# Kernel optimization log

Hardware: AMD Instinct MI355X
Metric: run time of the kernel (lower is better)

The kernel has to match this reference:

```python
import jax, jax.numpy as jnp
import numpy as np

B, Z, H, T = 256, 512, 2048, 16
EPS = 1e-5

def _normalize(v):
    return v / (jnp.linalg.norm(v) + 1e-12)

def setup_inputs() -> dict:
    key = jax.random.key(0)
    ks = jax.random.split(key, 10)
    s = lambda fan: 1.0 / np.sqrt(fan)
    return {
        "z": jax.random.normal(ks[0], (B, Z), dtype=jnp.float32),
        "fc_w": jax.random.normal(ks[1], (Z, Z), dtype=jnp.float32) * s(Z),
        "fc_b": jnp.zeros((Z,), dtype=jnp.float32),
        "fc_u": _normalize(jax.random.normal(ks[2], (Z,), dtype=jnp.float32)),
        "w_ih": jax.random.normal(ks[3], (3 * H, Z), dtype=jnp.float32) * s(Z),
        "w_hh": jax.random.normal(ks[4], (3 * H, H), dtype=jnp.float32) * s(H),
        "b_ih": jnp.zeros((3 * H,), dtype=jnp.float32).at[H:2 * H].set(1.0),  # forget-gate bias init
        "b_hh": jnp.zeros((3 * H,), dtype=jnp.float32),
        "lin_w": jax.random.normal(ks[5], (Z, H), dtype=jnp.float32) * s(H),
        "lin_b": jnp.zeros((Z,), dtype=jnp.float32),
    }

def _spectral_norm(w, u):
    # one torch-style power iteration (u, v treated as constants)
    v = jax.lax.stop_gradient(_normalize(w.T @ u))
    u1 = jax.lax.stop_gradient(_normalize(w @ v))
    sigma = u1 @ (w @ v)
    return w / sigma

def reference(z, fc_w, fc_b, fc_u, w_ih, w_hh, b_ih, b_hh, lin_w, lin_b):
    # spectral-norm linear: h0 = z @ (W/sigma)^T + b
    w_sn = _spectral_norm(fc_w, fc_u)
    x0 = z @ w_sn.T + fc_b                      # [B, Z]
    h0 = jnp.zeros((B, H), dtype=z.dtype)       # initHidden

    def step(carry, _):
        x, h = carry
        gi = x @ w_ih.T + b_ih                  # [B, 3H]
        gh = h @ w_hh.T + b_hh                  # [B, 3H]
        i_r, i_z, i_n = jnp.split(gi, 3, axis=1)
        h_r, h_z, h_n = jnp.split(gh, 3, axis=1)
        r = jax.nn.sigmoid(i_r + h_r)
        u = jax.nn.sigmoid(i_z + h_z)
        n = jnp.tanh(i_n + r * h_n)
        h_new = (1.0 - u) * n + u * h
        x_new = h_new @ lin_w.T + lin_b         # [B, Z] fed back as next input
        return (x_new, h_new), x_new

    _, outs = jax.lax.scan(step, (x0, h0), None, length=T)  # [T, B, Z]

    # per-timestep BatchNorm1d(affine=False), training-mode batch stats
    mean = jnp.mean(outs, axis=1, keepdims=True)
    var = jnp.mean((outs - mean) ** 2, axis=1, keepdims=True)
    y = (outs - mean) / jnp.sqrt(var + EPS)     # [T, B, Z]

    y = jnp.transpose(y, (1, 0, 2))             # [B, T, Z]
    return y.reshape(-1, Z)                     # [B*T, Z]
```

## Files before the change

kernel.cpp:

```cpp
#include <hip/hip_runtime.h>
#include <hip/hip_bf16.h>
#include <cstdint>
#include <cstddef>

#define B_  256
#define Z_  512
#define H_  2048
#define T_  16
#define H3_ 6144

using short8  = __attribute__((ext_vector_type(8))) short;
using bf16x8  = __attribute__((ext_vector_type(8))) __bf16;
using f32x4   = __attribute__((ext_vector_type(4))) float;
using f32x16  = __attribute__((ext_vector_type(16))) float;

__device__ __forceinline__ f32x4 mfma_bf16(short8 a, short8 b, f32x4 c) {
  return __builtin_amdgcn_mfma_f32_16x16x32_bf16(
      __builtin_bit_cast(bf16x8, a), __builtin_bit_cast(bf16x8, b), c, 0, 0, 0);
}
__device__ __forceinline__ f32x16 mfma_bf16_32(short8 a, short8 b, f32x16 c) {
  return __builtin_amdgcn_mfma_f32_32x32x16_bf16(
      __builtin_bit_cast(bf16x8, a), __builtin_bit_cast(bf16x8, b), c, 0, 0, 0);
}

__device__ __forceinline__ unsigned short f2bf(float f) {
  unsigned int u = __builtin_bit_cast(unsigned int, f);
  u = (u + 0x7FFFu + ((u >> 16) & 1u)) >> 16;
  return (unsigned short)u;
}

__device__ __forceinline__ float sigmoidf_(float x) { return 1.0f / (1.0f + __expf(-x)); }

__device__ __forceinline__ int swz(int row, int chunk) {
  return row * 64 + ((chunk ^ (row & 7)) << 3);
}

__global__ __launch_bounds__(512, 1) void gru_step4(
    const unsigned short* __restrict__ A, int K,
    const unsigned short* __restrict__ Wr,
    const unsigned short* __restrict__ Wz,
    const unsigned short* __restrict__ Wn,
    const unsigned short* __restrict__ Whn,
    const float* __restrict__ cr, const float* __restrict__ cz,
    const float* __restrict__ cn, const float* __restrict__ chn,
    float hn_scale,
    const float* __restrict__ h_old,
    float* __restrict__ h_new,
    unsigned short* __restrict__ h_hist)
{
  __shared__ __align__(16) unsigned short sbuf[2][12288];
  __shared__ float LDSf[4][64][33];
  const int bid = blockIdx.x, tid = threadIdx.x;
  const int xcd = bid & 7, rst = bid >> 3;
  const int m_idx = rst & 3, gg = rst >> 2;
  const int grp = gg * 8 + xcd;
  const int m0 = m_idx * 64;
  const int gh0 = grp * 32;
  const int wave = tid >> 6, lane = tid & 63;
  const int gate = wave & 3, mh = wave >> 2;
  const int lh = lane >> 5, l31 = lane & 31;

  const int arow = tid >> 3, achk = tid & 7;
  const int wrow = tid >> 2, wc0 = (tid & 3) * 2;
  const unsigned short* wsrc =
      (wrow < 32) ? Wr : (wrow < 64) ? Wz : (wrow < 96) ? Wn : Whn;
  const size_t aoff = (size_t)(m0 + arow) * K + achk * 8;
  const size_t woff = (size_t)(gh0 + (wrow & 31)) * K + wc0 * 8;
  const int sa_d  = swz(arow, achk);
  const int sw_d0 = 4096 + swz(wrow, wc0 + 0);
  const int sw_d1 = 4096 + swz(wrow, wc0 + 1);

  uint4 Aa, Aw0, Aw1;
  uint4 Ba, Bw0, Bw1;

#define LDSET(a, w0, w1, k0)                               \
  {                                                        \
    const int kk_ = (k0);                                  \
    a  = *(const uint4*)(A    + aoff + kk_);               \
    w0 = *(const uint4*)(wsrc + woff + kk_);               \
    w1 = *(const uint4*)(wsrc + woff + kk_ + 8);           \
  }
#define STAGE(s, a, w0, w1)                                \
  {                                                        \
    unsigned short* b_ = sbuf[s];                          \
    *(uint4*)(b_ + sa_d)  = a;                             \
    *(uint4*)(b_ + sw_d0) = w0;                            \
    *(uint4*)(b_ + sw_d1) = w1;                            \
  }

  f32x16 acc = {};
#define COMP(s)                                                            \
  {                                                                        \
    const unsigned short* b_ = sbuf[s];                                    \
    _Pragma("unroll")                                                      \
    for (int ks = 0; ks < 4; ++ks) {                                       \
      short8 af = *(const short8*)(b_ + swz(mh * 32 + l31, ks * 2 + lh));  \
      short8 wf = *(const short8*)(b_ + 4096 + swz(gate * 32 + l31, ks * 2 + lh)); \
      acc = mfma_bf16_32(af, wf, acc);                                     \
    }                                                                      \
  }

  const int nIter = K >> 6;
  LDSET(Aa, Aw0, Aw1, 0);
  LDSET(Ba, Bw0, Bw1, 64);
  for (int it = 0; it < nIter; it += 2) {
    STAGE(0, Aa, Aw0, Aw1);
    __syncthreads();
    { const int kn = (it + 2 < nIter) ? ((it + 2) << 6) : 0;
      LDSET(Aa, Aw0, Aw1, kn); }
    COMP(0);
    STAGE(1, Ba, Bw0, Bw1);
    __syncthreads();
    { const int kn = (it + 3 < nIter) ? ((it + 3) << 6) : 64;
      LDSET(Ba, Bw0, Bw1, kn); }
    COMP(1);
  }
#undef LDSET
#undef STAGE
#undef COMP

#pragma unroll
  for (int reg = 0; reg < 16; ++reg) {
    const int trow = (reg & 3) + 8 * (reg >> 2) + 4 * lh;
    LDSf[gate][mh * 32 + trow][l31] = acc[reg];
  }
  __syncthreads();
  {
    const int row = tid >> 3, c0 = (tid & 7) * 4;
    const int grow = m0 + row;
#pragma unroll
    for (int j = 0; j < 4; ++j) {
      const int col = c0 + j;
      const int gcol = gh0 + col;
      const float R   = sigmoidf_(LDSf[0][row][col] + cr[gcol]);
      const float U   = sigmoidf_(LDSf[1][row][col] + cz[gcol]);
      const float HNv = hn_scale * LDSf[3][row][col] + chn[gcol];
      const float Nv  = tanhf(LDSf[2][row][col] + cn[gcol] + R * HNv);
      const float ho  = h_old ? h_old[(size_t)grow * H_ + gcol] : 0.0f;
      const float hv  = (1.0f - U) * Nv + U * ho;
      h_new[(size_t)grow * H_ + gcol]  = hv;
      h_hist[(size_t)grow * H_ + gcol] = f2bf(hv);
    }
  }
}

__global__ __launch_bounds__(256) void gemm_bt(
    const unsigned short* __restrict__ A,
    const unsigned short* __restrict__ Bw,
    int K,
    const float* __restrict__ addsrc, int add_ld,
    const float* __restrict__ bias,
    const float* __restrict__ scale_ptr,
    unsigned short* __restrict__ out_bf,
    float* __restrict__ out_f, int ldo)
{
  __shared__ unsigned short sA[32 * 64];
  __shared__ unsigned short sB[64 * 64];
  const int tid  = threadIdx.x;
  const int m0   = blockIdx.x * 32, n0 = blockIdx.y * 64;
  const int wave = tid >> 6, lane = tid & 63;
  const int wr = wave & 1, wc = wave >> 1;
  const int q = lane >> 4, c16 = lane & 15;
  const int lr = tid >> 3, lc8 = tid & 7;
  f32x4 acc0 = {}, acc1 = {};
  const size_t rowA  = (size_t)(m0 + lr) * K;
  const size_t rowB0 = (size_t)(n0 + lr) * K;
  const size_t rowB1 = (size_t)(n0 + 32 + lr) * K;
  for (int k0 = 0; k0 < K; k0 += 64) {
    const int gc = k0 + lc8 * 8;
    uint4 ra  = *(const uint4*)(A  + rowA  + gc);
    uint4 rb0 = *(const uint4*)(Bw + rowB0 + gc);
    uint4 rb1 = *(const uint4*)(Bw + rowB1 + gc);
    __syncthreads();
    *(uint4*)(sA + swz(lr, lc8))      = ra;
    *(uint4*)(sB + swz(lr, lc8))      = rb0;
    *(uint4*)(sB + swz(32 + lr, lc8)) = rb1;
    __syncthreads();
#pragma unroll
    for (int kk = 0; kk < 2; ++kk) {
      const int arow = wr * 16 + c16;
      short8 af = *(const short8*)(sA + swz(arow, kk * 4 + q));
      const int brow = wc * 32 + c16;
      short8 b0 = *(const short8*)(sB + swz(brow, kk * 4 + q));
      acc0 = mfma_bf16(af, b0, acc0);
      short8 b1 = *(const short8*)(sB + swz(brow + 16, kk * 4 + q));
      acc1 = mfma_bf16(af, b1, acc1);
    }
  }
  const float scale = scale_ptr ? *scale_ptr : 1.0f;
#pragma unroll
  for (int cf = 0; cf < 2; ++cf) {
    f32x4 a = cf ? acc1 : acc0;
#pragma unroll
    for (int v = 0; v < 4; ++v) {
      const int row = m0 + wr * 16 + q * 4 + v;
      const int col = n0 + wc * 32 + cf * 16 + c16;
      float val = a[v] * scale;
      if (addsrc) val += addsrc[(size_t)row * add_ld + col];
      if (bias)   val += bias[col];
      if (out_f)  out_f[(size_t)row * ldo + col] = val;
      if (out_bf) out_bf[(size_t)row * ldo + col] = f2bf(val);
    }
  }
}

__global__ __launch_bounds__(256) void gemm_bt64(
    const unsigned short* __restrict__ A,
    const unsigned short* __restrict__ Bw,
    int K,
    const float* __restrict__ addsrc, int add_ld,
    const float* __restrict__ bias,
    unsigned short* __restrict__ out_bf,
    float* __restrict__ out_f, int ldo)
{
  __shared__ unsigned short sA[64 * 64];
  __shared__ unsigned short sB[64 * 64];
  const int tid  = threadIdx.x;
  const int m0   = blockIdx.x * 64, n0 = blockIdx.y * 64;
  const int wave = tid >> 6, lane = tid & 63;
  const int wr = wave & 1, wc = wave >> 1;
  const int q = lane >> 4, c16 = lane & 15;
  const int lr = tid >> 3, lc8 = tid & 7;
  f32x4 acc[2][2] = {};
  const size_t aoff = (size_t)(m0 + lr) * K;
  const size_t boff = (size_t)(n0 + lr) * K;
  const size_t s32  = (size_t)32 * K;

  uint4 ra0, ra1, rb0, rb1;
  auto LOAD = [&](int k0) {
    const int gc = k0 + lc8 * 8;
    ra0 = *(const uint4*)(A  + aoff + gc);
    ra1 = *(const uint4*)(A  + aoff + s32 + gc);
    rb0 = *(const uint4*)(Bw + boff + gc);
    rb1 = *(const uint4*)(Bw + boff + s32 + gc);
  };

  const int nIter = K >> 6;
  LOAD(0);
  for (int it = 0; it < nIter; ++it) {
    __syncthreads();
    *(uint4*)(sA + swz(lr, lc8))      = ra0;
    *(uint4*)(sA + swz(lr + 32, lc8)) = ra1;
    *(uint4*)(sB + swz(lr, lc8))      = rb0;
    *(uint4*)(sB + swz(lr + 32, lc8)) = rb1;
    __syncthreads();
    if (it + 1 < nIter) LOAD((it + 1) << 6);
#pragma unroll
    for (int kk = 0; kk < 2; ++kk) {
      short8 af0 = *(const short8*)(sA + swz(wr * 32 + c16,      kk * 4 + q));
      short8 af1 = *(const short8*)(sA + swz(wr * 32 + 16 + c16, kk * 4 + q));
      short8 bf0 = *(const short8*)(sB + swz(wc * 32 + c16,      kk * 4 + q));
      short8 bf1 = *(const short8*)(sB + swz(wc * 32 + 16 + c16, kk * 4 + q));
      acc[0][0] = mfma_bf16(af0, bf0, acc[0][0]);
      acc[0][1] = mfma_bf16(af0, bf1, acc[0][1]);
      acc[1][0] = mfma_bf16(af1, bf0, acc[1][0]);
      acc[1][1] = mfma_bf16(af1, bf1, acc[1][1]);
    }
  }
#pragma unroll
  for (int i = 0; i < 2; ++i) {
#pragma unroll
    for (int j = 0; j < 2; ++j) {
#pragma unroll
      for (int v = 0; v < 4; ++v) {
        const int row = m0 + wr * 32 + i * 16 + q * 4 + v;
        const int col = n0 + wc * 32 + j * 16 + c16;
        float val = acc[i][j][v];
        if (addsrc) val += addsrc[(size_t)row * add_ld + col];
        if (bias)   val += bias[col];
        if (out_f)  out_f[(size_t)row * ldo + col] = val;
        if (out_bf) out_bf[(size_t)row * ldo + col] = f2bf(val);
      }
    }
  }
}

__global__ __launch_bounds__(256) void quant_all(
    const float* __restrict__ z, const float* __restrict__ fc_w,
    const float* __restrict__ w_ih, const float* __restrict__ w_hh,
    const float* __restrict__ lin_w,
    unsigned short* __restrict__ z_q, unsigned short* __restrict__ fc_w_q,
    unsigned short* __restrict__ w_ih_q, unsigned short* __restrict__ w_hhn_q,
    unsigned short* __restrict__ lin_w_q)
{
  const int i = blockIdx.x * 256 + threadIdx.x;
  if (i >= 2195456) return;
  const float4* src; ushort4* dst; int idx;
  if (i < 32768)        { src = (const float4*)z;     dst = (ushort4*)z_q;     idx = i; }
  else if (i < 98304)   { src = (const float4*)fc_w;  dst = (ushort4*)fc_w_q;  idx = i - 32768; }
  else if (i < 884736)  { src = (const float4*)w_ih;  dst = (ushort4*)w_ih_q;  idx = i - 98304; }
  else if (i < 1933312) { src = (const float4*)(w_hh + (size_t)2 * H_ * H_);
                          dst = (ushort4*)w_hhn_q;    idx = i - 884736; }
  else                  { src = (const float4*)lin_w; dst = (ushort4*)lin_w_q; idx = i - 1933312; }
  float4 v = src[idx];
  ushort4 o; o.x = f2bf(v.x); o.y = f2bf(v.y); o.z = f2bf(v.z); o.w = f2bf(v.w);
  dst[idx] = o;
}

__global__ __launch_bounds__(256) void transq(const float* __restrict__ s,
                                              unsigned short* __restrict__ d) {
  __shared__ float tile[32][33];
  const int tx = threadIdx.x & 31, ty = threadIdx.x >> 5;
  const int k0 = blockIdx.x * 32, z0 = blockIdx.y * 32;
#pragma unroll
  for (int j = 0; j < 4; ++j)
    tile[ty + j * 8][tx] = s[(size_t)(z0 + ty + j * 8) * H_ + k0 + tx];
  __syncthreads();
#pragma unroll
  for (int j = 0; j < 4; ++j)
    d[(size_t)(k0 + ty + j * 8) * Z_ + z0 + tx] = f2bf(tile[tx][ty + j * 8]);
}

__global__ void sigma1(const float* __restrict__ W, const float* __restrict__ u,
                       float* __restrict__ t1) {
  __shared__ float part[4][64];
  const int lane = threadIdx.x & 63, wv = threadIdx.x >> 6;
  const int col = blockIdx.x * 64 + lane;
  float s = 0.f;
  for (int r = wv * 128; r < wv * 128 + 128; ++r)
    s += W[(size_t)r * Z_ + col] * u[r];
  part[wv][lane] = s;
  __syncthreads();
  if (wv == 0)
    t1[col] = part[0][lane] + part[1][lane] + part[2][lane] + part[3][lane];
}

__global__ void sigma1b(const float* __restrict__ t1, float* __restrict__ invn) {
  __shared__ float red[256];
  int t = threadIdx.x;
  float v0 = t1[t], v1 = t1[t + 256];
  red[t] = v0 * v0 + v1 * v1;
  __syncthreads();
  for (int s = 128; s > 0; s >>= 1) {
    if (t < s) red[t] += red[t + s];
    __syncthreads();
  }
  if (t == 0) invn[0] = 1.0f / (sqrtf(red[0]) + 1e-12f);
}

__global__ void sigma2(const float* __restrict__ W, const float* __restrict__ t1,
                       const float* __restrict__ invn, float* __restrict__ t2) {
  const int lane = threadIdx.x & 63, wv = threadIdx.x >> 6;
  const int row = blockIdx.x * 4 + wv;
  float s = 0.f;
  for (int c = lane; c < Z_; c += 64) s += W[(size_t)row * Z_ + c] * t1[c];
#pragma unroll
  for (int off = 32; off > 0; off >>= 1) s += __shfl_down(s, off);
  if (lane == 0) t2[row] = s * invn[0];
}

__global__ void sigma3(const float* __restrict__ t2, float* __restrict__ inv_sig) {
  __shared__ float red[256];
  int t = threadIdx.x;
  float v0 = t2[t], v1 = t2[t + 256];
  red[t] = v0 * v0 + v1 * v1;
  __syncthreads();
  for (int s = 128; s > 0; s >>= 1) {
    if (t < s) red[t] += red[t + s];
    __syncthreads();
  }
  if (t == 0) {
    float s2  = red[0];
    float sig = s2 / (sqrtf(s2) + 1e-12f);
    inv_sig[0] = 1.0f / sig;
  }
}

__global__ __launch_bounds__(256) void dots_k(const float* __restrict__ w,
                                              const float* __restrict__ lb,
                                              float* __restrict__ dvec) {
  const int wave = threadIdx.x >> 6, lane = threadIdx.x & 63;
#pragma unroll
  for (int i = 0; i < 4; ++i) {
    int row = blockIdx.x * 16 + wave * 4 + i;
    float s = 0.f;
    for (int c = lane; c < Z_; c += 64) s += w[(size_t)row * Z_ + c] * lb[c];
#pragma unroll
    for (int off = 32; off > 0; off >>= 1) s += __shfl_down(s, off);
    if (lane == 0) dvec[row] = s;
  }
}

__global__ void consts_k(const float* __restrict__ b_ih, const float* __restrict__ b_hh,
                         const float* __restrict__ dvec,
                         float* __restrict__ c0r, float* __restrict__ c0z,
                         float* __restrict__ c0n,
                         float* __restrict__ c1r, float* __restrict__ c1z,
                         float* __restrict__ c1n, float* __restrict__ chn) {
  int j = blockIdx.x * 256 + threadIdx.x;
  float br = b_ih[j], bz = b_ih[H_ + j], bn = b_ih[2 * H_ + j];
  float hr = b_hh[j], hz = b_hh[H_ + j], hn = b_hh[2 * H_ + j];
  c0r[j] = br + hr; c0z[j] = bz + hz; c0n[j] = bn; chn[j] = hn;
  c1r[j] = br + hr + dvec[j];
  c1z[j] = bz + hz + dvec[H_ + j];
  c1n[j] = bn + dvec[2 * H_ + j];
}

__global__ __launch_bounds__(256) void bn_k(const float* __restrict__ outs,
                                            float* __restrict__ y) {
  __shared__ float s_sum[4][64], s_sq[4][64], s_mean[64], s_inv[64];
  const int t = blockIdx.x, zb = blockIdx.y;
  const int zl = threadIdx.x & 63, bp = threadIdx.x >> 6;
  const int z = zb * 64 + zl;
  float sum = 0.f, sq = 0.f;
  for (int b = bp * 64; b < bp * 64 + 64; ++b) {
    float v = outs[(size_t)(t * 256 + b) * Z_ + z];
    sum += v; sq += v * v;
  }
  s_sum[bp][zl] = sum; s_sq[bp][zl] = sq;
  __syncthreads();
  if (bp == 0) {
    float S = s_sum[0][zl] + s_sum[1][zl] + s_sum[2][zl] + s_sum[3][zl];
    float Q = s_sq[0][zl] + s_sq[1][zl] + s_sq[2][zl] + s_sq[3][zl];
    float mean = S * (1.0f / 256.0f);
    float var  = Q * (1.0f / 256.0f) - mean * mean;
    s_mean[zl] = mean;
    s_inv[zl]  = rsqrtf(var + 1e-5f);
  }
  __syncthreads();
  const float mean = s_mean[zl], inv = s_inv[zl];
  for (int b = bp * 64; b < bp * 64 + 64; ++b) {
    float v = outs[(size_t)(t * 256 + b) * Z_ + z];
    y[(size_t)(b * T_ + t) * Z_ + z] = (v - mean) * inv;
  }
}

extern "C" void kernel_launch(void* const* d_in, const int* in_sizes, int n_in,
                              void* d_out, int out_size, void* d_ws, size_t ws_size,
                              hipStream_t stream) {
  const float* z     = (const float*)d_in[0];
  const float* fc_w  = (const float*)d_in[1];
  const float* fc_b  = (const float*)d_in[2];
  const float* fc_u  = (const float*)d_in[3];
  const float* w_ih  = (const float*)d_in[4];
  const float* w_hh  = (const float*)d_in[5];
  const float* b_ih  = (const float*)d_in[6];
  const float* b_hh  = (const float*)d_in[7];
  const float* lin_w = (const float*)d_in[8];
  const float* lin_b = (const float*)d_in[9];
  float* out = (float*)d_out;

  char* ws = (char*)d_ws;
  size_t off = 0;
  auto alloc = [&](size_t bytes) -> void* {
    off = (off + 255) & ~(size_t)255;
    void* p = ws + off;
    off += bytes;
    return p;
  };
  unsigned short* w_ih_q   = (unsigned short*)alloc((size_t)H3_ * Z_ * 2);
  unsigned short* w_hhn_q  = (unsigned short*)alloc((size_t)H_ * H_ * 2);
  unsigned short* lin_w_q  = (unsigned short*)alloc((size_t)Z_ * H_ * 2);
  unsigned short* lin_wT_q = (unsigned short*)alloc((size_t)Z_ * H_ * 2);
  unsigned short* fc_w_q   = (unsigned short*)alloc((size_t)Z_ * Z_ * 2);
  unsigned short* z_q      = (unsigned short*)alloc((size_t)B_ * Z_ * 2);
  unsigned short* x0_q     = (unsigned short*)alloc((size_t)B_ * Z_ * 2);
  unsigned short* Wsum_r   = (unsigned short*)alloc((size_t)H_ * H_ * 2);
  unsigned short* Wsum_z   = (unsigned short*)alloc((size_t)H_ * H_ * 2);
  unsigned short* Wn_c     = (unsigned short*)alloc((size_t)H_ * H_ * 2);
  unsigned short* Hhist    = (unsigned short*)alloc((size_t)T_ * B_ * H_ * 2);
  float* h_f32 = (float*)alloc((size_t)2 * B_ * H_ * 4);
  float* outs  = (float*)alloc((size_t)T_ * B_ * Z_ * 4);
  float* c0r = (float*)alloc(H_ * 4);
  float* c0z = (float*)alloc(H_ * 4);
  float* c0n = (float*)alloc(H_ * 4);
  float* c1r = (float*)alloc(H_ * 4);
  float* c1z = (float*)alloc(H_ * 4);
  float* c1n = (float*)alloc(H_ * 4);
  float* chn = (float*)alloc(H_ * 4);
  float* dvec = (float*)alloc(H3_ * 4);
  float* t1v = (float*)alloc(Z_ * 4);
  float* t2v = (float*)alloc(Z_ * 4);
  float* invn = (float*)alloc(256);
  float* invsig = (float*)alloc(256);
  (void)in_sizes; (void)n_in; (void)out_size; (void)ws_size;

  quant_all<<<dim3((2195456 + 255) / 256), 256, 0, stream>>>(
      z, fc_w, w_ih, w_hh, lin_w, z_q, fc_w_q, w_ih_q, w_hhn_q, lin_w_q);
  transq<<<dim3(64, 16), 256, 0, stream>>>(lin_w, lin_wT_q);
  sigma1<<<8, 256, 0, stream>>>(fc_w, fc_u, t1v);
  sigma1b<<<1, 256, 0, stream>>>(t1v, invn);
  sigma2<<<128, 256, 0, stream>>>(fc_w, t1v, invn, t2v);
  sigma3<<<1, 256, 0, stream>>>(t2v, invsig);
  dots_k<<<384, 256, 0, stream>>>(w_ih, lin_b, dvec);
  consts_k<<<8, 256, 0, stream>>>(b_ih, b_hh, dvec, c0r, c0z, c0n, c1r, c1z, c1n, chn);

  gemm_bt<<<dim3(B_ / 32, Z_ / 64), 256, 0, stream>>>(
      z_q, fc_w_q, Z_, nullptr, 0, fc_b, invsig, x0_q, nullptr, Z_);

  for (int g = 0; g < 3; ++g) {
    const float* adds = (g < 2) ? (w_hh + (size_t)g * H_ * H_) : nullptr;
    unsigned short* outw = (g == 0) ? Wsum_r : (g == 1) ? Wsum_z : Wn_c;
    gemm_bt64<<<dim3(H_ / 64, H_ / 64), 256, 0, stream>>>(
        w_ih_q + (size_t)g * H_ * Z_, lin_wT_q, Z_, adds, H_, nullptr,
        outw, nullptr, H_);
  }

  for (int t = 0; t < T_; ++t) {
    if (t == 0) {
      gru_step4<<<256, 512, 0, stream>>>(
          x0_q, Z_,
          w_ih_q, w_ih_q + (size_t)H_ * Z_, w_ih_q + (size_t)2 * H_ * Z_,
          w_ih_q ,
          c0r, c0z, c0n, chn, 0.0f, nullptr, h_f32, Hhist);
    } else {
      gru_step4<<<256, 512, 0, stream>>>(
          Hhist + (size_t)(t - 1) * B_ * H_, H_,
          Wsum_r, Wsum_z, Wn_c, w_hhn_q,
          c1r, c1z, c1n, chn, 1.0f,
          h_f32 + (size_t)((t - 1) & 1) * B_ * H_,
          h_f32 + (size_t)(t & 1) * B_ * H_,
          Hhist + (size_t)t * B_ * H_);
    }
  }

  gemm_bt64<<<dim3(T_ * B_ / 64, Z_ / 64), 256, 0, stream>>>(
      Hhist, lin_w_q, H_, nullptr, 0, lin_b, nullptr, outs, Z_);

  bn_k<<<dim3(T_, Z_ / 64), 256, 0, stream>>>(outs, out);
}
```

Baseline: 402.9 us.

## Split-K GRU step with 2x2 MFMA tiles, merge weight-sum GEMMs and setup kernels

The per-step GRU kernel now gives each of four k-slices to a wave group. Each wave computes a 2x2 block of 32x32 MFMA tiles, so A and W fragments are reused within the wave, and a shared-memory reduction sums the partial results. The three weight-sum GEMMs become one launch with 128x128 tiles. The sigma and bias-constant setup kernels are merged to cut launch count. The split-K reduction adds extra LDS traffic and a shared buffer of 96KB plus staging, which raises LDS pressure in exchange for fewer redundant fragment loads.

```diff
diff --git a/kernel.cpp b/kernel.cpp
--- a/kernel.cpp
+++ b/kernel.cpp
@@ -35,7 +35,7 @@
   return row * 64 + ((chunk ^ (row & 7)) << 3);
 }
 
-__global__ __launch_bounds__(512, 1) void gru_step4(
+__global__ __launch_bounds__(512, 1) void gru_step7(
     const unsigned short* __restrict__ A, int K,
     const unsigned short* __restrict__ Wr,
     const unsigned short* __restrict__ Wz,
@@ -49,7 +49,8 @@
     unsigned short* __restrict__ h_hist)
 {
   __shared__ __align__(16) unsigned short sbuf[2][12288];
-  __shared__ float LDSf[4][64][33];
+  __shared__ float red[6][4096];
+  float* LDSf = (float*)sbuf;
   const int bid = blockIdx.x, tid = threadIdx.x;
   const int xcd = bid & 7, rst = bid >> 3;
   const int m_idx = rst & 3, gg = rst >> 2;
@@ -57,7 +58,7 @@
   const int m0 = m_idx * 64;
   const int gh0 = grp * 32;
   const int wave = tid >> 6, lane = tid & 63;
-  const int gate = wave & 3, mh = wave >> 2;
+  const int s4 = wave & 3, gp = wave >> 2;
   const int lh = lane >> 5, l31 = lane & 31;
 
   const int arow = tid >> 3, achk = tid & 7;
@@ -88,16 +89,21 @@
     *(uint4*)(b_ + sw_d1) = w1;                            \
   }
 
-  f32x16 acc = {};
-#define COMP(s)                                                            \
+  f32x16 a00 = {}, a01 = {}, a10 = {}, a11 = {};
+  const int g0r = gp * 64, g1r = gp * 64 + 32;
+
+#define COMP(sb)                                                           \
   {                                                                        \
-    const unsigned short* b_ = sbuf[s];                                    \
-    _Pragma("unroll")                                                      \
-    for (int ks = 0; ks < 4; ++ks) {                                       \
-      short8 af = *(const short8*)(b_ + swz(mh * 32 + l31, ks * 2 + lh));  \
-      short8 wf = *(const short8*)(b_ + 4096 + swz(gate * 32 + l31, ks * 2 + lh)); \
-      acc = mfma_bf16_32(af, wf, acc);                                     \
-    }                                                                      \
+    const unsigned short* b_ = sbuf[sb];                                   \
+    const int ch = s4 * 2 + lh;                                            \
+    short8 af0 = *(const short8*)(b_ + swz(l31, ch));                      \
+    short8 af1 = *(const short8*)(b_ + swz(32 + l31, ch));                 \
+    short8 wf0 = *(const short8*)(b_ + 4096 + swz(g0r + l31, ch));         \
+    short8 wf1 = *(const short8*)(b_ + 4096 + swz(g1r + l31, ch));         \
+    a00 = mfma_bf16_32(af0, wf0, a00);                                     \
+    a01 = mfma_bf16_32(af0, wf1, a01);                                     \
+    a10 = mfma_bf16_32(af1, wf0, a10);                                     \
+    a11 = mfma_bf16_32(af1, wf1, a11);                                     \
   }
 
   const int nIter = K >> 6;
@@ -119,10 +125,41 @@
 #undef STAGE
 #undef COMP
 
-#pragma unroll
-  for (int reg = 0; reg < 16; ++reg) {
-    const int trow = (reg & 3) + 8 * (reg >> 2) + 4 * lh;
-    LDSf[gate][mh * 32 + trow][l31] = acc[reg];
+  __syncthreads();
+  if (s4 != 0) {
+    float* rp = red[(s4 - 1) * 2 + gp];
+#pragma unroll
+    for (int r = 0; r < 16; ++r) rp[(0 * 16 + r) * 64 + lane] = a00[r];
+#pragma unroll
+    for (int r = 0; r < 16; ++r) rp[(1 * 16 + r) * 64 + lane] = a01[r];
+#pragma unroll
+    for (int r = 0; r < 16; ++r) rp[(2 * 16 + r) * 64 + lane] = a10[r];
+#pragma unroll
+    for (int r = 0; r < 16; ++r) rp[(3 * 16 + r) * 64 + lane] = a11[r];
+  }
+  __syncthreads();
+  if (s4 == 0) {
+#pragma unroll
+    for (int ss = 0; ss < 3; ++ss) {
+      const float* rp = red[ss * 2 + gp];
+#pragma unroll
+      for (int r = 0; r < 16; ++r) a00[r] += rp[(0 * 16 + r) * 64 + lane];
+#pragma unroll
+      for (int r = 0; r < 16; ++r) a01[r] += rp[(1 * 16 + r) * 64 + lane];
+#pragma unroll
+      for (int r = 0; r < 16; ++r) a10[r] += rp[(2 * 16 + r) * 64 + lane];
+#pragma unroll
+      for (int r = 0; r < 16; ++r) a11[r] += rp[(3 * 16 + r) * 64 + lane];
+    }
+    const int gA = gp * 2, gB = gp * 2 + 1;
+#pragma unroll
+    for (int r = 0; r < 16; ++r) {
+      const int trow = (r & 3) + 8 * (r >> 2) + 4 * lh;
+      LDSf[(gA * 64 + trow     ) * 33 + l31] = a00[r];
+      LDSf[(gB * 64 + trow     ) * 33 + l31] = a01[r];
+      LDSf[(gA * 64 + 32 + trow) * 33 + l31] = a10[r];
+      LDSf[(gB * 64 + 32 + trow) * 33 + l31] = a11[r];
+    }
   }
   __syncthreads();
   {
@@ -132,14 +169,88 @@
     for (int j = 0; j < 4; ++j) {
       const int col = c0 + j;
       const int gcol = gh0 + col;
-      const float R   = sigmoidf_(LDSf[0][row][col] + cr[gcol]);
-      const float U   = sigmoidf_(LDSf[1][row][col] + cz[gcol]);
-      const float HNv = hn_scale * LDSf[3][row][col] + chn[gcol];
-      const float Nv  = tanhf(LDSf[2][row][col] + cn[gcol] + R * HNv);
+      const float R   = sigmoidf_(LDSf[(0 * 64 + row) * 33 + col] + cr[gcol]);
+      const float U   = sigmoidf_(LDSf[(1 * 64 + row) * 33 + col] + cz[gcol]);
+      const float HNv = hn_scale * LDSf[(3 * 64 + row) * 33 + col] + chn[gcol];
+      const float Nv  = tanhf(LDSf[(2 * 64 + row) * 33 + col] + cn[gcol] + R * HNv);
       const float ho  = h_old ? h_old[(size_t)grow * H_ + gcol] : 0.0f;
       const float hv  = (1.0f - U) * Nv + U * ho;
       h_new[(size_t)grow * H_ + gcol]  = hv;
       h_hist[(size_t)grow * H_ + gcol] = f2bf(hv);
+    }
+  }
+}
+
+__global__ __launch_bounds__(512) void gemm128_wsum(
+    const unsigned short* __restrict__ w_ih_q,
+    const unsigned short* __restrict__ lin_wT_q,
+    const float* __restrict__ w_hh,
+    unsigned short* __restrict__ Wsum_r,
+    unsigned short* __restrict__ Wsum_z,
+    unsigned short* __restrict__ Wn_c)
+{
+  __shared__ __align__(16) unsigned short sA[2][8192];
+  __shared__ __align__(16) unsigned short sB[2][8192];
+  const int g = blockIdx.y >> 4, nj = blockIdx.y & 15;
+  const unsigned short* Aq = w_ih_q + (size_t)g * H_ * Z_;
+  const float* adds = (g < 2) ? (w_hh + (size_t)g * H_ * H_) : nullptr;
+  unsigned short* outw = (g == 0) ? Wsum_r : (g == 1) ? Wsum_z : Wn_c;
+  const int K = Z_;
+  const int m0 = blockIdx.x * 128, n0 = nj * 128;
+  const int tid = threadIdx.x;
+  const int wave = tid >> 6, lane = tid & 63;
+  const int wr = wave & 1, wc = wave >> 1;
+  const int lh = lane >> 5, l31 = lane & 31;
+  const int srow = tid >> 2, sc0 = (tid & 3) * 2;
+  const size_t aoff = (size_t)(m0 + srow) * K + sc0 * 8;
+  const size_t boff = (size_t)(n0 + srow) * K + sc0 * 8;
+  const int sd0 = swz(srow, sc0), sd1 = swz(srow, sc0 + 1);
+  f32x16 acc0 = {}, acc1 = {};
+  uint4 A0, A1, B0, B1, C0, C1, D0, D1;
+#define LD(a0, a1, b0, b1, k0)                              \
+  { const int kk_ = (k0);                                   \
+    a0 = *(const uint4*)(Aq + aoff + kk_);                  \
+    a1 = *(const uint4*)(Aq + aoff + kk_ + 8);              \
+    b0 = *(const uint4*)(lin_wT_q + boff + kk_);            \
+    b1 = *(const uint4*)(lin_wT_q + boff + kk_ + 8); }
+#define ST(s, a0, a1, b0, b1)                               \
+  { *(uint4*)(sA[s] + sd0) = a0; *(uint4*)(sA[s] + sd1) = a1; \
+    *(uint4*)(sB[s] + sd0) = b0; *(uint4*)(sB[s] + sd1) = b1; }
+#define CP(s)                                               \
+  { _Pragma("unroll")                                       \
+    for (int ks = 0; ks < 4; ++ks) {                        \
+      const int ch = ks * 2 + lh;                           \
+      short8 af0 = *(const short8*)(sA[s] + swz(wr * 64 + l31, ch));      \
+      short8 af1 = *(const short8*)(sA[s] + swz(wr * 64 + 32 + l31, ch)); \
+      short8 bf  = *(const short8*)(sB[s] + swz(wc * 32 + l31, ch));      \
+      acc0 = mfma_bf16_32(af0, bf, acc0);                   \
+      acc1 = mfma_bf16_32(af1, bf, acc1); } }
+  const int nIter = K >> 6;
+  LD(A0, A1, B0, B1, 0);
+  LD(C0, C1, D0, D1, 64);
+  for (int it = 0; it < nIter; it += 2) {
+    ST(0, A0, A1, B0, B1);
+    __syncthreads();
+    { const int kn = (it + 2 < nIter) ? ((it + 2) << 6) : 0; LD(A0, A1, B0, B1, kn); }
+    CP(0);
+    ST(1, C0, C1, D0, D1);
+    __syncthreads();
+    { const int kn = (it + 3 < nIter) ? ((it + 3) << 6) : 64; LD(C0, C1, D0, D1, kn); }
+    CP(1);
+  }
+#undef LD
+#undef ST
+#undef CP
+#pragma unroll
+  for (int i = 0; i < 2; ++i) {
+    const f32x16 a = i ? acc1 : acc0;
+#pragma unroll
+    for (int r = 0; r < 16; ++r) {
+      const int row = m0 + wr * 64 + i * 32 + (r & 3) + 8 * (r >> 2) + 4 * lh;
+      const int col = n0 + wc * 32 + l31;
+      float val = a[r];
+      if (adds) val += adds[(size_t)row * H_ + col];
+      outw[(size_t)row * H_ + col] = f2bf(val);
     }
   }
 }
@@ -325,28 +436,26 @@
     t1[col] = part[0][lane] + part[1][lane] + part[2][lane] + part[3][lane];
 }
 
-__global__ void sigma1b(const float* __restrict__ t1, float* __restrict__ invn) {
+__global__ void sigma2(const float* __restrict__ W, const float* __restrict__ t1,
+                       float* __restrict__ t2) {
   __shared__ float red[256];
-  int t = threadIdx.x;
-  float v0 = t1[t], v1 = t1[t + 256];
-  red[t] = v0 * v0 + v1 * v1;
+  const int tid = threadIdx.x;
+  float p = 0.f;
+  for (int c = tid; c < Z_; c += 256) { float v = t1[c]; p += v * v; }
+  red[tid] = p;
   __syncthreads();
   for (int s = 128; s > 0; s >>= 1) {
-    if (t < s) red[t] += red[t + s];
-    __syncthreads();
-  }
-  if (t == 0) invn[0] = 1.0f / (sqrtf(red[0]) + 1e-12f);
-}
-
-__global__ void sigma2(const float* __restrict__ W, const float* __restrict__ t1,
-                       const float* __restrict__ invn, float* __restrict__ t2) {
-  const int lane = threadIdx.x & 63, wv = threadIdx.x >> 6;
+    if (tid < s) red[tid] += red[tid + s];
+    __syncthreads();
+  }
+  const float invn = 1.0f / (sqrtf(red[0]) + 1e-12f);
+  const int lane = tid & 63, wv = tid >> 6;
   const int row = blockIdx.x * 4 + wv;
   float s = 0.f;
   for (int c = lane; c < Z_; c += 64) s += W[(size_t)row * Z_ + c] * t1[c];
 #pragma unroll
   for (int off = 32; off > 0; off >>= 1) s += __shfl_down(s, off);
-  if (lane == 0) t2[row] = s * invn[0];
+  if (lane == 0) t2[row] = s * invn;
 }
 
 __global__ void sigma3(const float* __restrict__ t2, float* __restrict__ inv_sig) {
@@ -366,9 +475,13 @@
   }
 }
 
-__global__ __launch_bounds__(256) void dots_k(const float* __restrict__ w,
-                                              const float* __restrict__ lb,
-                                              float* __restrict__ dvec) {
+__global__ __launch_bounds__(256) void dots2_k(
+    const float* __restrict__ w, const float* __restrict__ lb,
+    const float* __restrict__ b_ih, const float* __restrict__ b_hh,
+    float* __restrict__ c0r, float* __restrict__ c0z, float* __restrict__ c0n,
+    float* __restrict__ c1r, float* __restrict__ c1z, float* __restrict__ c1n,
+    float* __restrict__ chn)
+{
   const int wave = threadIdx.x >> 6, lane = threadIdx.x & 63;
 #pragma unroll
   for (int i = 0; i < 4; ++i) {
@@ -377,23 +490,14 @@
     for (int c = lane; c < Z_; c += 64) s += w[(size_t)row * Z_ + c] * lb[c];
 #pragma unroll
     for (int off = 32; off > 0; off >>= 1) s += __shfl_down(s, off);
-    if (lane == 0) dvec[row] = s;
-  }
-}
-
-__global__ void consts_k(const float* __restrict__ b_ih, const float* __restrict__ b_hh,
-                         const float* __restrict__ dvec,
-                         float* __restrict__ c0r, float* __restrict__ c0z,
-                         float* __restrict__ c0n,
-                         float* __restrict__ c1r, float* __restrict__ c1z,
-                         float* __restrict__ c1n, float* __restrict__ chn) {
-  int j = blockIdx.x * 256 + threadIdx.x;
-  float br = b_ih[j], bz = b_ih[H_ + j], bn = b_ih[2 * H_ + j];
-  float hr = b_hh[j], hz = b_hh[H_ + j], hn = b_hh[2 * H_ + j];
-  c0r[j] = br + hr; c0z[j] = bz + hz; c0n[j] = bn; chn[j] = hn;
-  c1r[j] = br + hr + dvec[j];
-  c1z[j] = bz + hz + dvec[H_ + j];
-  c1n[j] = bn + dvec[2 * H_ + j];
+    if (lane == 0) {
+      const int g = row >> 11, j = row & 2047;
+      const float bi = b_ih[row], bh = b_hh[row];
+      if (g == 0)      { c0r[j] = bi + bh; c1r[j] = bi + bh + s; }
+      else if (g == 1) { c0z[j] = bi + bh; c1z[j] = bi + bh + s; }
+      else             { c0n[j] = bi;      c1n[j] = bi + s;      chn[j] = bh; }
+    }
+  }
 }
 
 __global__ __launch_bounds__(256) void bn_k(const float* __restrict__ outs,
@@ -468,10 +572,8 @@
   float* c1z = (float*)alloc(H_ * 4);
   float* c1n = (float*)alloc(H_ * 4);
   float* chn = (float*)alloc(H_ * 4);
-  float* dvec = (float*)alloc(H3_ * 4);
   float* t1v = (float*)alloc(Z_ * 4);
   float* t2v = (float*)alloc(Z_ * 4);
-  float* invn = (float*)alloc(256);
   float* invsig = (float*)alloc(256);
   (void)in_sizes; (void)n_in; (void)out_size; (void)ws_size;
 
@@ -479,32 +581,26 @@
       z, fc_w, w_ih, w_hh, lin_w, z_q, fc_w_q, w_ih_q, w_hhn_q, lin_w_q);
   transq<<<dim3(64, 16), 256, 0, stream>>>(lin_w, lin_wT_q);
   sigma1<<<8, 256, 0, stream>>>(fc_w, fc_u, t1v);
-  sigma1b<<<1, 256, 0, stream>>>(t1v, invn);
-  sigma2<<<128, 256, 0, stream>>>(fc_w, t1v, invn, t2v);
+  sigma2<<<128, 256, 0, stream>>>(fc_w, t1v, t2v);
   sigma3<<<1, 256, 0, stream>>>(t2v, invsig);
-  dots_k<<<384, 256, 0, stream>>>(w_ih, lin_b, dvec);
-  consts_k<<<8, 256, 0, stream>>>(b_ih, b_hh, dvec, c0r, c0z, c0n, c1r, c1z, c1n, chn);
+  dots2_k<<<384, 256, 0, stream>>>(w_ih, lin_b, b_ih, b_hh,
+                                   c0r, c0z, c0n, c1r, c1z, c1n, chn);
 
   gemm_bt<<<dim3(B_ / 32, Z_ / 64), 256, 0, stream>>>(
       z_q, fc_w_q, Z_, nullptr, 0, fc_b, invsig, x0_q, nullptr, Z_);
 
-  for (int g = 0; g < 3; ++g) {
-    const float* adds = (g < 2) ? (w_hh + (size_t)g * H_ * H_) : nullptr;
-    unsigned short* outw = (g == 0) ? Wsum_r : (g == 1) ? Wsum_z : Wn_c;
-    gemm_bt64<<<dim3(H_ / 64, H_ / 64), 256, 0, stream>>>(
-        w_ih_q + (size_t)g * H_ * Z_, lin_wT_q, Z_, adds, H_, nullptr,
-        outw, nullptr, H_);
-  }
+  gemm128_wsum<<<dim3(H_ / 128, 48), 512, 0, stream>>>(
+      w_ih_q, lin_wT_q, w_hh, Wsum_r, Wsum_z, Wn_c);
 
   for (int t = 0; t < T_; ++t) {
     if (t == 0) {
-      gru_step4<<<256, 512, 0, stream>>>(
+      gru_step7<<<256, 512, 0, stream>>>(
           x0_q, Z_,
           w_ih_q, w_ih_q + (size_t)H_ * Z_, w_ih_q + (size_t)2 * H_ * Z_,
           w_ih_q ,
           c0r, c0z, c0n, chn, 0.0f, nullptr, h_f32, Hhist);
     } else {
-      gru_step4<<<256, 512, 0, stream>>>(
+      gru_step7<<<256, 512, 0, stream>>>(
           Hhist + (size_t)(t - 1) * B_ * H_, H_,
           Wsum_r, Wsum_z, Wn_c, w_hhn_q,
           c1r, c1z, c1n, chn, 1.0f,
```

After: 411.4 us. 1.02x slower.
